# Optimization experiments

Hardware: AMD Instinct MI355X
Metric: run time of the kernel (lower is better)

## Reference

```python
import jax, jax.numpy as jnp
import numpy as np

LATENT = 128
DISC = 64
RNN = 512
CODE = 512
INPUT = 2


def _lstm_cell(x, h, c, Wih, Whh, bih, bhh):
    # PyTorch LSTMCell: gate order (i, f, g, o)
    gates = x @ Wih.T + h @ Whh.T + bih + bhh
    i, f, g, o = jnp.split(gates, 4, axis=-1)
    c_new = jax.nn.sigmoid(f) * c + jax.nn.sigmoid(i) * jnp.tanh(g)
    h_new = jax.nn.sigmoid(o) * jnp.tanh(c_new)
    return h_new, c_new


def setup_inputs() -> dict:
    key = jax.random.key(0)
    ks = jax.random.split(key, 12)
    B = 4096
    s = lambda *sh: 1.0 / np.sqrt(sh[-1])
    inp = {
        'latent': jax.random.normal(ks[0], (B, LATENT), dtype=jnp.float32),
        'W_unpack': jax.random.normal(ks[1], (CODE, LATENT + INPUT), dtype=jnp.float32) * s(CODE, LATENT + INPUT),
        'b_unpack': jnp.zeros((CODE,), dtype=jnp.float32),
        'Wih0': jax.random.normal(ks[2], (4 * RNN, CODE), dtype=jnp.float32) * s(4 * RNN, CODE),
        'Whh0': jax.random.normal(ks[3], (4 * RNN, RNN), dtype=jnp.float32) * s(4 * RNN, RNN),
        'bih0': jnp.zeros((4 * RNN,), dtype=jnp.float32),
        'bhh0': jnp.zeros((4 * RNN,), dtype=jnp.float32),
        'Wih1': jax.random.normal(ks[4], (4 * RNN, RNN), dtype=jnp.float32) * s(4 * RNN, RNN),
        'Whh1': jax.random.normal(ks[5], (4 * RNN, RNN), dtype=jnp.float32) * s(4 * RNN, RNN),
        'bih1': jnp.zeros((4 * RNN,), dtype=jnp.float32),
        'bhh1': jnp.zeros((4 * RNN,), dtype=jnp.float32),
        'W_angle': jax.random.normal(ks[6], (DISC, RNN), dtype=jnp.float32) * s(DISC, RNN),
        'b_angle': jnp.zeros((DISC,), dtype=jnp.float32),
        'num_segments': 64,
    }
    return inp


def reference(latent, W_unpack, b_unpack, Wih0, Whh0, bih0, bhh0,
              Wih1, Whh1, bih1, bhh1, W_angle, b_angle, num_segments):
    B = latent.shape[0]
    space = jnp.linspace(-1.0, 1.0, DISC, dtype=latent.dtype)  # [DISC]
    # fixed gumbel noise for all steps: [S, B, DISC]
    u = jax.random.uniform(jax.random.key(42), (num_segments, B, DISC),
                           dtype=latent.dtype, minval=1e-8, maxval=1.0)
    gumbels = -jnp.log(-jnp.log(u))

    def step(carry, g):
        prev, h0, c0, h1, c1 = carry
        x = jnp.tanh(jnp.concatenate([latent, prev], axis=-1) @ W_unpack.T + b_unpack)
        h0, c0 = _lstm_cell(x, h0, c0, Wih0, Whh0, bih0, bhh0)
        h1, c1 = _lstm_cell(h0, h1, c1, Wih1, Whh1, bih1, bhh1)
        logits = h1 @ W_angle.T + b_angle
        # gumbel-softmax, tau=1 (torch default), hard=True with straight-through
        y_soft = jax.nn.softmax(logits + g, axis=-1)
        y_hard = jax.nn.one_hot(jnp.argmax(y_soft, axis=-1), DISC, dtype=y_soft.dtype)
        y = y_soft + jax.lax.stop_gradient(y_hard - y_soft)
        angles = jnp.sum(y * space, axis=-1, keepdims=True)  # [B,1]
        seg = jnp.concatenate([angles, jnp.zeros_like(angles)], axis=-1)  # [B,2]
        return (seg, h0, c0, h1, c1), seg

    z = jnp.zeros((B, RNN), dtype=latent.dtype)
    init = (jnp.zeros((B, INPUT), dtype=latent.dtype), z, z, z, z)
    _, segs = jax.lax.scan(step, init, gumbels)  # [S, B, 2]
    return jnp.transpose(segs, (1, 0, 2))  # [B, S, 2]
```

## Files before the change

kernel.cpp:

```cpp
#include <hip/hip_runtime.h>
#include <cstdint>

#define BATCH 4096
#define LATENT 128
#define RNN 512
#define CODE 512
#define DISC 64
#define NSEG 64
#define UNPACK_COLS 130

__device__ __forceinline__ uint32_t rotl32(uint32_t x, uint32_t r) {
  return (x << r) | (x >> (32u - r));
}

__device__ __forceinline__ uint32_t threefry_bits(uint32_t n) {
  const uint32_t k0 = 0u, k1 = 42u;
  const uint32_t ks2 = k0 ^ k1 ^ 0x1BD11BDAu;
  uint32_t x0 = 0u, x1 = n;
  x0 += k0; x1 += k1;
#define TF_ROUND(r) { x0 += x1; x1 = rotl32(x1, r); x1 ^= x0; }
  TF_ROUND(13) TF_ROUND(15) TF_ROUND(26) TF_ROUND(6)
  x0 += k1;  x1 += ks2 + 1u;
  TF_ROUND(17) TF_ROUND(29) TF_ROUND(16) TF_ROUND(24)
  x0 += ks2; x1 += k0 + 2u;
  TF_ROUND(13) TF_ROUND(15) TF_ROUND(26) TF_ROUND(6)
  x0 += k0;  x1 += k1 + 3u;
  TF_ROUND(17) TF_ROUND(29) TF_ROUND(16) TF_ROUND(24)
  x0 += k1;  x1 += ks2 + 4u;
  TF_ROUND(13) TF_ROUND(15) TF_ROUND(26) TF_ROUND(6)
  x0 += ks2; x1 += k0 + 5u;
#undef TF_ROUND
  return x0 ^ x1;
}

__device__ __forceinline__ float sigmoidf_(float v) {
  return 1.0f / (1.0f + expf(-v));
}

__global__ __launch_bounds__(256) void base_kernel(
    const float* __restrict__ latent, const float* __restrict__ Wu,
    const float* __restrict__ bu, float* __restrict__ base) {
  __shared__ float lrow[LATENT];
  const int b = blockIdx.x;
  if (threadIdx.x < LATENT) lrow[threadIdx.x] = latent[b * LATENT + threadIdx.x];
  __syncthreads();
  for (int n = threadIdx.x; n < CODE; n += 256) {
    const float* wr = Wu + (size_t)n * UNPACK_COLS;
    float acc = 0.f;
#pragma unroll 8
    for (int k = 0; k < LATENT; ++k) acc += lrow[k] * wr[k];
    base[(size_t)b * CODE + n] = acc + bu[n];
  }
}

__global__ __launch_bounds__(256) void x_kernel(
    const float* __restrict__ base, const float* __restrict__ angle,
    const float* __restrict__ Wu, float* __restrict__ xo) {
  const int idx = blockIdx.x * 256 + threadIdx.x;
  const int b = idx >> 9;
  const int n = idx & 511;
  xo[idx] = tanhf(base[idx] + angle[b] * Wu[(size_t)n * UNPACK_COLS + 128]);
}

#define BMW 64
#define KSTEP 16

__global__ __launch_bounds__(512, 2) void gemm_lstm(
    const float* __restrict__ A1, const float* __restrict__ W1,
    const float* __restrict__ A2, const float* __restrict__ W2,
    const float* __restrict__ b1, const float* __restrict__ b2,
    float* __restrict__ c_io, float* __restrict__ h_out) {
  __shared__ __align__(16) float Ws[KSTEP][512];
  const int tid = threadIdx.x;
  const int lane = tid & 63;
  const int wv = tid >> 6;
  const int d = blockIdx.x;
  const int bx = (d & 7) >> 1;
  const int by = ((d >> 3) << 1) | (d & 1);
  const int rowBase = by * BMW;

  const int wn = ((tid >> 7) * RNN) + (bx << 7) + (tid & 127);
  const float* __restrict__ wrow1 = W1 + (size_t)wn * RNN;
  const float* __restrict__ wrow2 = W2 + (size_t)wn * RNN;

  float acc[8][8];
#pragma unroll
  for (int i = 0; i < 8; ++i)
#pragma unroll
    for (int j = 0; j < 8; ++j) acc[i][j] = 0.f;

  for (int seg = 0; seg < 2; ++seg) {
    const float* __restrict__ A = seg ? A2 : A1;
    const float* __restrict__ wrow = seg ? wrow2 : wrow1;
    float4 st[4];
#pragma unroll
    for (int q = 0; q < 4; ++q) st[q] = *(const float4*)&wrow[q * 4];

    for (int k0 = 0; k0 < RNN; k0 += KSTEP) {
      __syncthreads();
#pragma unroll
      for (int q = 0; q < 4; ++q) {
        Ws[q * 4 + 0][tid] = st[q].x;
        Ws[q * 4 + 1][tid] = st[q].y;
        Ws[q * 4 + 2][tid] = st[q].z;
        Ws[q * 4 + 3][tid] = st[q].w;
      }
      __syncthreads();
      if (k0 + KSTEP < RNN) {
#pragma unroll
        for (int q = 0; q < 4; ++q)
          st[q] = *(const float4*)&wrow[k0 + KSTEP + q * 4];
      }
      const float* __restrict__ abase = A + (size_t)(rowBase + wv * 8) * RNN + k0;
#pragma unroll
      for (int c4 = 0; c4 < 4; ++c4) {
        float4 af[8];
#pragma unroll
        for (int i = 0; i < 8; ++i)
          af[i] = *(const float4*)&abase[(size_t)i * RNN + c4 * 4];
        float4 wfA[4], wfB[4];
#pragma unroll
        for (int kk = 0; kk < 4; ++kk) {
          wfA[kk] = *(const float4*)&Ws[c4 * 4 + kk][4 * lane];
          wfB[kk] = *(const float4*)&Ws[c4 * 4 + kk][256 + 4 * lane];
        }
#pragma unroll
        for (int kk = 0; kk < 4; ++kk) {
#pragma unroll
          for (int i = 0; i < 8; ++i) {
            const float a = ((const float*)&af[i])[kk];
            acc[i][0] += a * wfA[kk].x;
            acc[i][1] += a * wfA[kk].y;
            acc[i][2] += a * wfA[kk].z;
            acc[i][3] += a * wfA[kk].w;
            acc[i][4] += a * wfB[kk].x;
            acc[i][5] += a * wfB[kk].y;
            acc[i][6] += a * wfB[kk].z;
            acc[i][7] += a * wfB[kk].w;
          }
        }
      }
    }
  }

  const int col0 = (bx << 7) + 4 * (lane & 31);
  const int gA = lane >> 5;
  const int gB = 2 + gA;
  float bsA[4], bsB[4];
#pragma unroll
  for (int j = 0; j < 4; ++j) {
    bsA[j] = b1[gA * RNN + col0 + j] + b2[gA * RNN + col0 + j];
    bsB[j] = b1[gB * RNN + col0 + j] + b2[gB * RNN + col0 + j];
  }
  const bool low = (lane < 32);
#pragma unroll
  for (int i = 0; i < 8; ++i) {
    float vA[4], vB[4], pA[4], pB[4];
#pragma unroll
    for (int j = 0; j < 4; ++j) {
      vA[j] = acc[i][j] + bsA[j];
      vB[j] = acc[i][4 + j] + bsB[j];
      pA[j] = __shfl_xor(vA[j], 32);
      pB[j] = __shfl_xor(vB[j], 32);
    }
    const bool mine = low ? (i < 4) : (i >= 4);
    if (mine) {
      const int row = rowBase + wv * 8 + i;
      const size_t off = (size_t)row * RNN + col0;
      const float4 cold = *(const float4*)&c_io[off];
      const float co[4] = {cold.x, cold.y, cold.z, cold.w};
      float cn[4], hn[4];
#pragma unroll
      for (int j = 0; j < 4; ++j) {
        const float fi = low ? vA[j] : pA[j];
        const float ff = low ? pA[j] : vA[j];
        const float fg = low ? vB[j] : pB[j];
        const float fo = low ? pB[j] : vB[j];
        const float c2 = sigmoidf_(ff) * co[j] + sigmoidf_(fi) * tanhf(fg);
        cn[j] = c2;
        hn[j] = sigmoidf_(fo) * tanhf(c2);
      }
      *(float4*)&c_io[off] = make_float4(cn[0], cn[1], cn[2], cn[3]);
      *(float4*)&h_out[off] = make_float4(hn[0], hn[1], hn[2], hn[3]);
    }
  }
}

__global__ __launch_bounds__(64) void head_kernel(
    const float* __restrict__ h1, const float* __restrict__ Wang,
    const float* __restrict__ bang, float* __restrict__ angle,
    float* __restrict__ out, int s) {
  const int b = blockIdx.x;
  const int d = threadIdx.x;
  const float4* hr = (const float4*)(h1 + (size_t)b * RNN);
  const float4* wr = (const float4*)(Wang + (size_t)d * RNN);
  float acc = 0.f;
#pragma unroll 16
  for (int k = 0; k < RNN / 4; ++k) {
    float4 a = hr[k], w = wr[k];
    acc += a.x * w.x; acc += a.y * w.y; acc += a.z * w.z; acc += a.w * w.w;
  }
  float z = acc + bang[d];
  const uint32_t n = ((uint32_t)s * BATCH + (uint32_t)b) * DISC + (uint32_t)d;
  const uint32_t bits = threefry_bits(n);
  const float f = __uint_as_float((bits >> 9) | 0x3f800000u) - 1.0f;
  const float u = fmaxf(1e-8f, f + 1e-8f);
  const float gum = -logf(-logf(u));
  z += gum;
  float m = z;
#pragma unroll
  for (int off = 32; off; off >>= 1) m = fmaxf(m, __shfl_xor(m, off));
  const float e = expf(z - m);
  float ssum = e;
#pragma unroll
  for (int off = 32; off; off >>= 1) ssum += __shfl_xor(ssum, off);
  const float y = e / ssum;
  float ymax = y;
#pragma unroll
  for (int off = 32; off; off >>= 1) ymax = fmaxf(ymax, __shfl_xor(ymax, off));
  const unsigned long long mask = __ballot(y == ymax);
  const int k = __ffsll(mask) - 1;
  if (d == 0) {
    const float sp = -1.0f + (2.0f / 63.0f) * (float)k;
    angle[b] = sp;
    out[((size_t)b * NSEG + s) * 2 + 0] = sp;
    out[((size_t)b * NSEG + s) * 2 + 1] = 0.0f;
  }
}

extern "C" void kernel_launch(void* const* d_in, const int* in_sizes, int n_in,
                              void* d_out, int out_size, void* d_ws, size_t ws_size,
                              hipStream_t stream) {
  const float* latent   = (const float*)d_in[0];
  const float* W_unpack = (const float*)d_in[1];
  const float* b_unpack = (const float*)d_in[2];
  const float* Wih0     = (const float*)d_in[3];
  const float* Whh0     = (const float*)d_in[4];
  const float* bih0     = (const float*)d_in[5];
  const float* bhh0     = (const float*)d_in[6];
  const float* Wih1     = (const float*)d_in[7];
  const float* Whh1     = (const float*)d_in[8];
  const float* bih1     = (const float*)d_in[9];
  const float* bhh1     = (const float*)d_in[10];
  const float* W_angle  = (const float*)d_in[11];
  const float* b_angle  = (const float*)d_in[12];
  float* out = (float*)d_out;

  const size_t HC = (size_t)BATCH * RNN;
  float* ws    = (float*)d_ws;
  float* h0a   = ws;
  float* h1a   = h0a + HC;
  float* c0    = h1a + HC;
  float* c1    = c0 + HC;
  float* angle = c1 + HC;
  float* h0b   = angle + BATCH;
  float* h1b   = h0b + HC;
  float* x     = h1b + HC;
  float* base  = x + (size_t)BATCH * CODE;

  hipMemsetAsync(ws, 0, (4 * HC + BATCH) * sizeof(float), stream);

  base_kernel<<<BATCH, 256, 0, stream>>>(latent, W_unpack, b_unpack, base);

  for (int s = 0; s < NSEG; ++s) {
    const int p = s & 1;
    float* h0p = p ? h0b : h0a; float* h0n = p ? h0a : h0b;
    float* h1p = p ? h1b : h1a; float* h1n = p ? h1a : h1b;
    x_kernel<<<(BATCH * CODE) / 256, 256, 0, stream>>>(base, angle, W_unpack, x);
    gemm_lstm<<<256, 512, 0, stream>>>(x, Wih0, h0p, Whh0, bih0, bhh0, c0, h0n);
    gemm_lstm<<<256, 512, 0, stream>>>(h0n, Wih1, h1p, Whh1, bih1, bhh1, c1, h1n);
    head_kernel<<<BATCH, 64, 0, stream>>>(h1n, W_angle, b_angle, angle, out, s);
  }
}
```

Before: 41.67 ms.

## Shrink LSTM GEMM tiles to 32 rows with register-double-buffered A prefetch

The fused LSTM gate GEMM now runs 256-thread blocks on a 4x128 grid, each covering 32 batch rows instead of 64, so there are twice as many smaller blocks. A-operand fragments are double-buffered in registers with software prefetch across k-steps. Weight tiles are loaded per k-step as coalesced float4 rows and transposed into shared memory. The aim is better occupancy and hiding of global-load latency. In exchange, each weight tile is reused across fewer rows, which doubles weight traffic per output, and the extra buffers raise register pressure.

Result: slower. 161.7 ms (+288.1%).

```diff
diff --git a/kernel.cpp b/kernel.cpp
--- a/kernel.cpp
+++ b/kernel.cpp
@@ -62,26 +62,30 @@
   xo[idx] = tanhf(base[idx] + angle[b] * Wu[(size_t)n * UNPACK_COLS + 128]);
 }
 
-#define BMW 64
-#define KSTEP 16
-
-__global__ __launch_bounds__(512, 2) void gemm_lstm(
+__global__ __launch_bounds__(256, 2) void gemm_lstm(
     const float* __restrict__ A1, const float* __restrict__ W1,
     const float* __restrict__ A2, const float* __restrict__ W2,
     const float* __restrict__ b1, const float* __restrict__ b2,
     float* __restrict__ c_io, float* __restrict__ h_out) {
-  __shared__ __align__(16) float Ws[KSTEP][512];
+  __shared__ __align__(16) float Ws[16 * 512];
   const int tid = threadIdx.x;
-  const int lane = tid & 63;
+  const int l = tid & 63;
   const int wv = tid >> 6;
-  const int d = blockIdx.x;
-  const int bx = (d & 7) >> 1;
-  const int by = ((d >> 3) << 1) | (d & 1);
-  const int rowBase = by * BMW;
-
-  const int wn = ((tid >> 7) * RNN) + (bx << 7) + (tid & 127);
-  const float* __restrict__ wrow1 = W1 + (size_t)wn * RNN;
-  const float* __restrict__ wrow2 = W2 + (size_t)wn * RNN;
+  const int bx = blockIdx.x;
+  const int rowBase = blockIdx.y * 32;
+  const int g0 = l >> 5;
+
+  int wrow[2][4];
+#pragma unroll
+  for (int c = 0; c < 2; ++c)
+#pragma unroll
+    for (int r = 0; r < 4; ++r) {
+      const int t = 256 * c + 4 * l + r;
+      wrow[c][r] = ((t >> 7) * RNN) + (bx << 7) + (t & 127);
+    }
+
+  const float* __restrict__ a1base = A1 + (size_t)(rowBase + wv * 8) * RNN;
+  const float* __restrict__ a2base = A2 + (size_t)(rowBase + wv * 8) * RNN;
 
   float acc[8][8];
 #pragma unroll
@@ -89,70 +93,78 @@
 #pragma unroll
     for (int j = 0; j < 8; ++j) acc[i][j] = 0.f;
 
+  float4 afA[8], afB[8];
+
+#define PF(dst, tn)                                                            \
+  {                                                                            \
+    if ((tn) < 256) {                                                          \
+      const float* __restrict__ bp = ((tn)&128) ? a2base : a1base;             \
+      const int off = (((tn) >> 2) & 31) * 16 + ((tn)&3) * 4;                  \
+      _Pragma("unroll") for (int i = 0; i < 8; ++i)                            \
+          dst[i] = *(const float4*)&bp[(size_t)i * RNN + off];                 \
+    }                                                                          \
+  }
+
+#define COMPUTE_C4(buf, c4)                                                    \
+  {                                                                            \
+    _Pragma("unroll") for (int kk = 0; kk < 4; ++kk) {                         \
+      const int krow = ((c4)*4 + kk) * 512;                                    \
+      const float4 wA = *(const float4*)&Ws[krow + g0 * 128 + 4 * (l & 31)];   \
+      const float4 wB =                                                        \
+          *(const float4*)&Ws[krow + 256 + g0 * 128 + 4 * (l & 31)];           \
+      _Pragma("unroll") for (int i = 0; i < 8; ++i) {                          \
+        const float a = ((const float*)&buf[i])[kk];                           \
+        acc[i][0] += a * wA.x; acc[i][1] += a * wA.y;                          \
+        acc[i][2] += a * wA.z; acc[i][3] += a * wA.w;                          \
+        acc[i][4] += a * wB.x; acc[i][5] += a * wB.y;                          \
+        acc[i][6] += a * wB.z; acc[i][7] += a * wB.w;                          \
+      }                                                                        \
+    }                                                                          \
+  }
+
+  PF(afA, 0)
+  int t = 0;
   for (int seg = 0; seg < 2; ++seg) {
-    const float* __restrict__ A = seg ? A2 : A1;
-    const float* __restrict__ wrow = seg ? wrow2 : wrow1;
-    float4 st[4];
-#pragma unroll
-    for (int q = 0; q < 4; ++q) st[q] = *(const float4*)&wrow[q * 4];
-
-    for (int k0 = 0; k0 < RNN; k0 += KSTEP) {
+    const float* __restrict__ Wseg = seg ? W2 : W1;
+    for (int k0 = 0; k0 < RNN; k0 += 16) {
+      float4 gw[2][4];
+#pragma unroll
+      for (int c = 0; c < 2; ++c)
+#pragma unroll
+        for (int r = 0; r < 4; ++r)
+          gw[c][r] = *(const float4*)&Wseg[(size_t)wrow[c][r] * RNN + k0 + 4 * wv];
       __syncthreads();
 #pragma unroll
-      for (int q = 0; q < 4; ++q) {
-        Ws[q * 4 + 0][tid] = st[q].x;
-        Ws[q * 4 + 1][tid] = st[q].y;
-        Ws[q * 4 + 2][tid] = st[q].z;
-        Ws[q * 4 + 3][tid] = st[q].w;
-      }
+      for (int c = 0; c < 2; ++c)
+#pragma unroll
+        for (int j = 0; j < 4; ++j) {
+          *(float4*)&Ws[(4 * wv + j) * 512 + 256 * c + 4 * l] =
+              make_float4(((const float*)&gw[c][0])[j],
+                          ((const float*)&gw[c][1])[j],
+                          ((const float*)&gw[c][2])[j],
+                          ((const float*)&gw[c][3])[j]);
+        }
       __syncthreads();
-      if (k0 + KSTEP < RNN) {
-#pragma unroll
-        for (int q = 0; q < 4; ++q)
-          st[q] = *(const float4*)&wrow[k0 + KSTEP + q * 4];
-      }
-      const float* __restrict__ abase = A + (size_t)(rowBase + wv * 8) * RNN + k0;
-#pragma unroll
-      for (int c4 = 0; c4 < 4; ++c4) {
-        float4 af[8];
-#pragma unroll
-        for (int i = 0; i < 8; ++i)
-          af[i] = *(const float4*)&abase[(size_t)i * RNN + c4 * 4];
-        float4 wfA[4], wfB[4];
-#pragma unroll
-        for (int kk = 0; kk < 4; ++kk) {
-          wfA[kk] = *(const float4*)&Ws[c4 * 4 + kk][4 * lane];
-          wfB[kk] = *(const float4*)&Ws[c4 * 4 + kk][256 + 4 * lane];
-        }
-#pragma unroll
-        for (int kk = 0; kk < 4; ++kk) {
-#pragma unroll
-          for (int i = 0; i < 8; ++i) {
-            const float a = ((const float*)&af[i])[kk];
-            acc[i][0] += a * wfA[kk].x;
-            acc[i][1] += a * wfA[kk].y;
-            acc[i][2] += a * wfA[kk].z;
-            acc[i][3] += a * wfA[kk].w;
-            acc[i][4] += a * wfB[kk].x;
-            acc[i][5] += a * wfB[kk].y;
-            acc[i][6] += a * wfB[kk].z;
-            acc[i][7] += a * wfB[kk].w;
-          }
-        }
-      }
-    }
-  }
-
-  const int col0 = (bx << 7) + 4 * (lane & 31);
-  const int gA = lane >> 5;
-  const int gB = 2 + gA;
+      PF(afB, t + 1) COMPUTE_C4(afA, 0)
+      PF(afA, t + 2) COMPUTE_C4(afB, 1)
+      PF(afB, t + 3) COMPUTE_C4(afA, 2)
+      PF(afA, t + 4) COMPUTE_C4(afB, 3)
+      t += 4;
+    }
+  }
+#undef PF
+#undef COMPUTE_C4
+
+  const int col0 = (bx << 7) + 4 * (l & 31);
+  const int gA = g0;
+  const int gB = 2 + g0;
   float bsA[4], bsB[4];
 #pragma unroll
   for (int j = 0; j < 4; ++j) {
     bsA[j] = b1[gA * RNN + col0 + j] + b2[gA * RNN + col0 + j];
     bsB[j] = b1[gB * RNN + col0 + j] + b2[gB * RNN + col0 + j];
   }
-  const bool low = (lane < 32);
+  const bool low = (l < 32);
 #pragma unroll
   for (int i = 0; i < 8; ++i) {
     float vA[4], vB[4], pA[4], pB[4];
@@ -262,13 +274,14 @@
 
   base_kernel<<<BATCH, 256, 0, stream>>>(latent, W_unpack, b_unpack, base);
 
+  dim3 ggrid(4, 128);
   for (int s = 0; s < NSEG; ++s) {
     const int p = s & 1;
     float* h0p = p ? h0b : h0a; float* h0n = p ? h0a : h0b;
     float* h1p = p ? h1b : h1a; float* h1n = p ? h1a : h1b;
     x_kernel<<<(BATCH * CODE) / 256, 256, 0, stream>>>(base, angle, W_unpack, x);
-    gemm_lstm<<<256, 512, 0, stream>>>(x, Wih0, h0p, Whh0, bih0, bhh0, c0, h0n);
-    gemm_lstm<<<256, 512, 0, stream>>>(h0n, Wih1, h1p, Whh1, bih1, bhh1, c1, h1n);
+    gemm_lstm<<<ggrid, 256, 0, stream>>>(x, Wih0, h0p, Whh0, bih0, bhh0, c0, h0n);
+    gemm_lstm<<<ggrid, 256, 0, stream>>>(h0n, Wih1, h1p, Whh1, bih1, bhh1, c1, h1n);
     head_kernel<<<BATCH, 64, 0, stream>>>(h1n, W_angle, b_angle, angle, out, s);
   }
 }
```
